# Kernel optimization log

Hardware: AMD Instinct MI355X
Metric: run time of the kernel (lower is better)

Reference implementation:

```python
import jax, jax.numpy as jnp
import numpy as np

EMBED_DIM = 1024
NUM_HEADS = 16
HEAD_DIM = 64
B, S = 4, 2048


def setup_inputs() -> dict:
    key = jax.random.key(0)
    ks = jax.random.split(key, 5)
    std = 0.02
    x = jax.random.normal(ks[0], (B, S, EMBED_DIM), dtype=jnp.float32)
    Wq = std * jax.random.normal(ks[1], (NUM_HEADS, EMBED_DIM, HEAD_DIM), dtype=jnp.float32)
    Wk = std * jax.random.normal(ks[2], (NUM_HEADS, EMBED_DIM, HEAD_DIM), dtype=jnp.float32)
    Wv = std * jax.random.normal(ks[3], (NUM_HEADS, EMBED_DIM, HEAD_DIM), dtype=jnp.float32)
    Wo = std * jax.random.normal(ks[4], (NUM_HEADS, HEAD_DIM, EMBED_DIM), dtype=jnp.float32)
    bq = jnp.zeros((NUM_HEADS, HEAD_DIM), dtype=jnp.float32)
    bk = jnp.zeros((NUM_HEADS, HEAD_DIM), dtype=jnp.float32)
    bv = jnp.zeros((NUM_HEADS, HEAD_DIM), dtype=jnp.float32)
    bo = jnp.zeros((EMBED_DIM,), dtype=jnp.float32)
    return {"x": x, "Wq": Wq, "bq": bq, "Wk": Wk, "bk": bk,
            "Wv": Wv, "bv": bv, "Wo": Wo, "bo": bo}


def reference(x, Wq, bq, Wk, bk, Wv, bv, Wo, bo):
    # q,k,v: [b, s, n, h]
    q = jnp.einsum('bsd,ndh->bsnh', x, Wq) + bq
    k = jnp.einsum('bsd,ndh->bsnh', x, Wk) + bk
    v = jnp.einsum('bsd,ndh->bsnh', x, Wv) + bv
    scale = 1.0 / (HEAD_DIM ** 0.5)
    # non-causal full attention matrix [b, n, s, t]
    attn = jnp.einsum('bsnh,btnh->bnst', q, k) * scale
    attn = jax.nn.softmax(attn, axis=-1)
    after = jnp.einsum('bnst,btnh->bsnh', attn, v)
    out = jnp.einsum('bsnh,nhd->bsd', after, Wo) + bo
    return out
```

## Files before the change

kernel.cpp:

```cpp
#include <hip/hip_runtime.h>

typedef __bf16 bf16;
typedef bf16 bf16x8 __attribute__((ext_vector_type(8)));
typedef bf16 bf16x4 __attribute__((ext_vector_type(4)));
typedef float f32x4 __attribute__((ext_vector_type(4)));

constexpr int Bb = 4, Ss = 2048, Dd = 1024, NH = 16, HD = 64;
constexpr int BS = Bb * Ss;
constexpr float CSC = 0.18033688011112042f;

__device__ __forceinline__ int sw(int row, int col) {
  return (row << 6) + (col ^ ((row & 7) << 3));
}

__device__ __forceinline__ void g2l16(const bf16* g, bf16* l) {
  __builtin_amdgcn_global_load_lds(
      (const __attribute__((address_space(1))) void*)g,
      (__attribute__((address_space(3))) void*)l, 16, 0, 0);
}

__global__ void convert_x(const float* __restrict__ x, bf16* __restrict__ xb) {
  int o = (blockIdx.x * 256 + threadIdx.x) * 4;
  f32x4 v = *(const f32x4*)&x[o];
  bf16x4 r = {(bf16)v[0], (bf16)v[1], (bf16)v[2], (bf16)v[3]};
  *(bf16x4*)&xb[o] = r;
}

__global__ void prep(const float* __restrict__ Wq, const float* __restrict__ Wk,
                     const float* __restrict__ Wv, const float* __restrict__ Wo,
                     const float* __restrict__ bq, const float* __restrict__ bk,
                     const float* __restrict__ bv,
                     bf16* __restrict__ WT_all, bf16* __restrict__ WoT,
                     float* __restrict__ bias_all) {
  __shared__ bf16 Ts[64 * 72];
  const int t = threadIdx.x;
  const int sel = blockIdx.y;
  if (sel < 3) {
    const float* W = (sel == 0) ? Wq : (sel == 1) ? Wk : Wv;
    float scale = (sel == 0) ? CSC : 1.0f;
    int head = blockIdx.x >> 4, dt = blockIdx.x & 15;
    const float* src = W + head * 65536 + dt * 64 * 64;
#pragma unroll
    for (int i = 0; i < 4; ++i) {
      int idx = i * 256 + t;
      int dr = idx >> 4, hc = (idx & 15) * 4;
      f32x4 v = *(const f32x4*)&src[dr * 64 + hc];
#pragma unroll
      for (int k = 0; k < 4; ++k) Ts[(hc + k) * 72 + dr] = (bf16)(v[k] * scale);
    }
    __syncthreads();
    bf16* dst = WT_all + (size_t)sel * 1048576 + (size_t)(head * 64) * 1024 + dt * 64;
#pragma unroll
    for (int i = 0; i < 2; ++i) {
      int idx = i * 256 + t;
      int hr = idx >> 3, ch = (idx & 7) * 8;
      *(bf16x8*)&dst[(size_t)hr * 1024 + ch] = *(const bf16x8*)&Ts[hr * 72 + ch];
    }
  } else if (sel == 3) {
    int ct = blockIdx.x >> 4, dt = blockIdx.x & 15;
    const float* src = Wo + (size_t)(ct * 64) * 1024 + dt * 64;
#pragma unroll
    for (int i = 0; i < 4; ++i) {
      int idx = i * 256 + t;
      int cr = idx >> 4, dc = (idx & 15) * 4;
      f32x4 v = *(const f32x4*)&src[(size_t)cr * 1024 + dc];
#pragma unroll
      for (int k = 0; k < 4; ++k) Ts[(dc + k) * 72 + cr] = (bf16)v[k];
    }
    __syncthreads();
    bf16* dst = WoT + (size_t)(dt * 64) * 1024 + ct * 64;
#pragma unroll
    for (int i = 0; i < 2; ++i) {
      int idx = i * 256 + t;
      int dr = idx >> 3, ch = (idx & 7) * 8;
      *(bf16x8*)&dst[(size_t)dr * 1024 + ch] = *(const bf16x8*)&Ts[dr * 72 + ch];
    }
  } else if (blockIdx.x == 0) {
    for (int j = t; j < 3072; j += 256) {
      int s2 = j >> 10;
      const float* bb = (s2 == 0) ? bq : (s2 == 1) ? bk : bv;
      bias_all[j] = bb[j & 1023] * (s2 == 0 ? CSC : 1.0f);
    }
  }
}

template <int EPI>
__global__ __launch_bounds__(256) void gemm128(const bf16* __restrict__ A,
                                               const bf16* __restrict__ BT,
                                               const float* __restrict__ bias,
                                               void* __restrict__ Cv, int ldc) {
  __shared__ __align__(16) bf16 As[128 * 64];
  __shared__ __align__(16) bf16 Bs[128 * 64];
  const int t = threadIdx.x;
  const int l = t & 63, q = l >> 4, lm = l & 15;
  const int w = t >> 6, wm = w & 1, wn = w >> 1;
  const int m0 = blockIdx.x * 128, n0 = blockIdx.y * 128;
  constexpr int K = 1024;
  int ro[4], co[4];
#pragma unroll
  for (int i = 0; i < 4; ++i) {
    int o = i * 256 + t;
    ro[i] = o >> 3;
    co[i] = ((o & 7) ^ ((o >> 3) & 7)) << 3;
  }
  const int lbase = (t & 192) * 8;
  f32x4 acc[4][4] = {};
  for (int k0 = 0; k0 < K; k0 += 64) {
    __syncthreads();
#pragma unroll
    for (int i = 0; i < 4; ++i)
      g2l16(&A[(size_t)(m0 + ro[i]) * K + k0 + co[i]], &As[i * 2048 + lbase]);
#pragma unroll
    for (int i = 0; i < 4; ++i)
      g2l16(&BT[(size_t)(n0 + ro[i]) * K + k0 + co[i]], &Bs[i * 2048 + lbase]);
    __syncthreads();
#pragma unroll
    for (int kh = 0; kh < 2; ++kh) {
      bf16x8 a[4], b[4];
#pragma unroll
      for (int i = 0; i < 4; ++i)
        a[i] = *(const bf16x8*)&As[sw(wm * 64 + i * 16 + lm, kh * 32 + q * 8)];
#pragma unroll
      for (int i = 0; i < 4; ++i)
        b[i] = *(const bf16x8*)&Bs[sw(wn * 64 + i * 16 + lm, kh * 32 + q * 8)];
#pragma unroll
      for (int mt = 0; mt < 4; ++mt)
#pragma unroll
        for (int nt = 0; nt < 4; ++nt)
          acc[mt][nt] = __builtin_amdgcn_mfma_f32_16x16x32_bf16(a[mt], b[nt], acc[mt][nt], 0, 0, 0);
    }
  }
  if (EPI == 1) {
    bf16* VT = (bf16*)Cv;
#pragma unroll
    for (int nt = 0; nt < 4; ++nt) {
      int sg = n0 + wn * 64 + nt * 16 + lm;
      size_t sb = (size_t)(sg >> 11) * 2097152 + (sg & 2047);
#pragma unroll
      for (int mt = 0; mt < 4; ++mt)
#pragma unroll
        for (int r = 0; r < 4; ++r) {
          int m = m0 + wm * 64 + mt * 16 + q * 4 + r;
          VT[sb + (size_t)(m >> 6) * 131072 + (size_t)(m & 63) * 2048] =
              (bf16)(acc[mt][nt][r] + bias[m]);
        }
    }
  } else {
#pragma unroll
    for (int nt = 0; nt < 4; ++nt) {
      int col = n0 + wn * 64 + nt * 16 + lm;
      float bb = bias[col];
#pragma unroll
      for (int mt = 0; mt < 4; ++mt) {
        int row = m0 + wm * 64 + mt * 16 + q * 4;
#pragma unroll
        for (int r = 0; r < 4; ++r) {
          if (EPI == 2)
            ((float*)Cv)[(size_t)(row + r) * ldc + col] = acc[mt][nt][r] + bb;
          else
            ((bf16*)Cv)[(size_t)(row + r) * ldc + col] = (bf16)(acc[mt][nt][r] + bb);
        }
      }
    }
  }
}

__global__ __launch_bounds__(256, 3) void attn(const bf16* __restrict__ QK,
                                               const bf16* __restrict__ VT,
                                               bf16* __restrict__ after) {
  __shared__ __align__(16) bf16 Ks[2][64 * 64];
  __shared__ __align__(16) bf16 Vs[2][64 * 64];
  __shared__ __align__(16) bf16 Ps[128 * 72];
  const int t = threadIdx.x;
  const int l = t & 63, q = l >> 4, lm = l & 15, w = t >> 6;
  const int f = blockIdx.x;
  const int bn = (f & 7) | ((f >> 7) << 3);
  const int s0 = ((f >> 3) & 15) * 128;
  const int b = bn >> 4, n = bn & 15;
  const bf16* Qb = QK + (size_t)(b * 2048) * 2048 + n * 64;
  const bf16* Kb = Qb + 1024;
  const bf16* Vtb = VT + (size_t)bn * 131072;
  int ro[4], co[4];
#pragma unroll
  for (int i = 0; i < 4; ++i) {
    int o = i * 256 + t;
    ro[i] = o >> 3;
    co[i] = ((o & 7) ^ ((o >> 3) & 7)) << 3;
  }
  const int lbase = (t & 192) * 8;
  bf16* Kflat = &Ks[0][0];
#pragma unroll
  for (int i = 0; i < 4; ++i)
    g2l16(&Qb[(size_t)(s0 + ro[i]) * 2048 + co[i]], Kflat + i * 2048 + lbase);
  __syncthreads();
  bf16x8 qa[2][2];
#pragma unroll
  for (int mt = 0; mt < 2; ++mt)
#pragma unroll
    for (int kh = 0; kh < 2; ++kh)
      qa[mt][kh] = *(const bf16x8*)&Kflat[sw(w * 32 + mt * 16 + lm, kh * 32 + q * 8)];
  __syncthreads();
#pragma unroll
  for (int i = 0; i < 2; ++i) {
    g2l16(&Kb[(size_t)ro[i] * 2048 + co[i]], &Ks[0][i * 2048 + lbase]);
    g2l16(&Vtb[(size_t)ro[i] * 2048 + co[i]], &Vs[0][i * 2048 + lbase]);
  }
  f32x4 o_acc[2][4] = {};
  f32x4 rsum[2] = {};
  const bf16x8 ones = {(bf16)1.f, (bf16)1.f, (bf16)1.f, (bf16)1.f,
                       (bf16)1.f, (bf16)1.f, (bf16)1.f, (bf16)1.f};
  for (int rd = 0; rd < 32; ++rd) {
    const int cur = rd & 1;
    __syncthreads();
    if (rd < 31) {
      int t0n = (rd + 1) * 64, nb = cur ^ 1;
#pragma unroll
      for (int i = 0; i < 2; ++i) {
        g2l16(&Kb[(size_t)(t0n + ro[i]) * 2048 + co[i]], &Ks[nb][i * 2048 + lbase]);
        g2l16(&Vtb[(size_t)ro[i] * 2048 + t0n + co[i]], &Vs[nb][i * 2048 + lbase]);
      }
    }
    f32x4 sc[2][4] = {};
#pragma unroll
    for (int kh = 0; kh < 2; ++kh) {
      bf16x8 kb[4];
#pragma unroll
      for (int c = 0; c < 4; ++c)
        kb[c] = *(const bf16x8*)&Ks[cur][sw(c * 16 + lm, kh * 32 + q * 8)];
#pragma unroll
      for (int mt = 0; mt < 2; ++mt)
#pragma unroll
        for (int c = 0; c < 4; ++c)
          sc[mt][c] = __builtin_amdgcn_mfma_f32_16x16x32_bf16(kb[c], qa[mt][kh], sc[mt][c], 0, 0, 0);
    }
#pragma unroll
    for (int mt = 0; mt < 2; ++mt) {
      int srow = w * 32 + mt * 16 + lm;
#pragma unroll
      for (int c = 0; c < 4; ++c) {
        bf16x4 pk;
#pragma unroll
        for (int r = 0; r < 4; ++r)
          pk[r] = (bf16)__builtin_amdgcn_exp2f(sc[mt][c][r]);
        *(bf16x4*)&Ps[srow * 72 + (c * 4 + q) * 4] = pk;
      }
    }
#pragma unroll
    for (int kh = 0; kh < 2; ++kh) {
      bf16x8 pa[2], vb[4];
#pragma unroll
      for (int mt = 0; mt < 2; ++mt)
        pa[mt] = *(const bf16x8*)&Ps[(w * 32 + mt * 16 + lm) * 72 + (kh * 8 + q * 2) * 4];
#pragma unroll
      for (int c = 0; c < 4; ++c)
        vb[c] = *(const bf16x8*)&Vs[cur][sw(c * 16 + lm, kh * 32 + q * 8)];
#pragma unroll
      for (int mt = 0; mt < 2; ++mt)
        rsum[mt] = __builtin_amdgcn_mfma_f32_16x16x32_bf16(pa[mt], ones, rsum[mt], 0, 0, 0);
#pragma unroll
      for (int mt = 0; mt < 2; ++mt)
#pragma unroll
        for (int c = 0; c < 4; ++c)
          o_acc[mt][c] = __builtin_amdgcn_mfma_f32_16x16x32_bf16(pa[mt], vb[c], o_acc[mt][c], 0, 0, 0);
    }
  }
#pragma unroll
  for (int mt = 0; mt < 2; ++mt)
#pragma unroll
    for (int r = 0; r < 4; ++r) {
      float inv = 1.f / rsum[mt][r];
      int srow = s0 + w * 32 + mt * 16 + q * 4 + r;
      size_t base = (size_t)(b * 2048 + srow) * 1024 + n * 64;
#pragma unroll
      for (int c = 0; c < 4; ++c)
        after[base + c * 16 + lm] = (bf16)(o_acc[mt][c][r] * inv);
    }
}

extern "C" void kernel_launch(void* const* d_in, const int* in_sizes, int n_in,
                              void* d_out, int out_size, void* d_ws, size_t ws_size,
                              hipStream_t stream) {
  const float* x  = (const float*)d_in[0];
  const float* Wq = (const float*)d_in[1];
  const float* bq = (const float*)d_in[2];
  const float* Wk = (const float*)d_in[3];
  const float* bk = (const float*)d_in[4];
  const float* Wv = (const float*)d_in[5];
  const float* bv = (const float*)d_in[6];
  const float* Wo = (const float*)d_in[7];
  const float* bo = (const float*)d_in[8];
  float* out = (float*)d_out;

  bf16* WT_all    = (bf16*)d_ws;
  bf16* WoT       = WT_all + (size_t)3072 * 1024;
  float* bias_all = (float*)(WoT + (size_t)1024 * 1024);
  bf16* xb        = (bf16*)(bias_all + 4096);
  bf16* QKb       = xb + (size_t)BS * Dd;
  bf16* VTb       = QKb + (size_t)BS * 2048;
  bf16* after     = VTb + (size_t)Bb * NH * HD * Ss;

  convert_x<<<dim3(BS * Dd / 1024), dim3(256), 0, stream>>>(x, xb);
  prep<<<dim3(256, 5), dim3(256), 0, stream>>>(Wq, Wk, Wv, Wo, bq, bk, bv,
                                               WT_all, WoT, bias_all);
  gemm128<0><<<dim3(64, 16), dim3(256), 0, stream>>>(xb, WT_all, bias_all, QKb, 2048);
  gemm128<1><<<dim3(8, 64), dim3(256), 0, stream>>>(WT_all + (size_t)2048 * 1024, xb,
                                                    bias_all + 2048, VTb, 0);
  attn<<<dim3(1024), dim3(256), 0, stream>>>(QKb, VTb, after);
  gemm128<2><<<dim3(64, 8), dim3(256), 0, stream>>>(after, WoT, bo, out, 1024);
}
```

Before: 290.5 us.

## Merge QK and V projection GEMMs into one launch with XCD-aware tile mapping

Fuses the separate QK and V projection GEMM launches into a single 1536-block kernel. Block indices are remapped so that blocks on the same XCD (bid&7) share weight column tiles, which should improve L2 reuse. The output GEMM gets the same XCD-aware mapping. The attention P-tile stride shrinks from 72 to 68, with P fragments read as two 8-byte loads to change the LDS bank pattern, at the cost of more LDS instructions.

```diff
diff --git a/kernel.cpp b/kernel.cpp
--- a/kernel.cpp
+++ b/kernel.cpp
@@ -8,6 +8,7 @@
 constexpr int Bb = 4, Ss = 2048, Dd = 1024, NH = 16, HD = 64;
 constexpr int BS = Bb * Ss;
 constexpr float CSC = 0.18033688011112042f;
+constexpr int PST = 68;
 
 __device__ __forceinline__ int sw(int row, int col) {
   return (row << 6) + (col ^ ((row & 7) << 3));
@@ -84,18 +85,13 @@
   }
 }
 
-template <int EPI>
-__global__ __launch_bounds__(256) void gemm128(const bf16* __restrict__ A,
-                                               const bf16* __restrict__ BT,
-                                               const float* __restrict__ bias,
-                                               void* __restrict__ Cv, int ldc) {
-  __shared__ __align__(16) bf16 As[128 * 64];
-  __shared__ __align__(16) bf16 Bs[128 * 64];
+__device__ __forceinline__ void gemm_core(const bf16* __restrict__ A,
+                                          const bf16* __restrict__ BT,
+                                          int m0, int n0, bf16* As, bf16* Bs,
+                                          f32x4 (&acc)[4][4]) {
   const int t = threadIdx.x;
   const int l = t & 63, q = l >> 4, lm = l & 15;
   const int w = t >> 6, wm = w & 1, wn = w >> 1;
-  const int m0 = blockIdx.x * 128, n0 = blockIdx.y * 128;
-  constexpr int K = 1024;
   int ro[4], co[4];
 #pragma unroll
   for (int i = 0; i < 4; ++i) {
@@ -104,15 +100,14 @@
     co[i] = ((o & 7) ^ ((o >> 3) & 7)) << 3;
   }
   const int lbase = (t & 192) * 8;
-  f32x4 acc[4][4] = {};
-  for (int k0 = 0; k0 < K; k0 += 64) {
+  for (int k0 = 0; k0 < 1024; k0 += 64) {
     __syncthreads();
 #pragma unroll
     for (int i = 0; i < 4; ++i)
-      g2l16(&A[(size_t)(m0 + ro[i]) * K + k0 + co[i]], &As[i * 2048 + lbase]);
+      g2l16(&A[(size_t)(m0 + ro[i]) * 1024 + k0 + co[i]], &As[i * 2048 + lbase]);
 #pragma unroll
     for (int i = 0; i < 4; ++i)
-      g2l16(&BT[(size_t)(n0 + ro[i]) * K + k0 + co[i]], &Bs[i * 2048 + lbase]);
+      g2l16(&BT[(size_t)(n0 + ro[i]) * 1024 + k0 + co[i]], &Bs[i * 2048 + lbase]);
     __syncthreads();
 #pragma unroll
     for (int kh = 0; kh < 2; ++kh) {
@@ -130,8 +125,37 @@
           acc[mt][nt] = __builtin_amdgcn_mfma_f32_16x16x32_bf16(a[mt], b[nt], acc[mt][nt], 0, 0, 0);
     }
   }
-  if (EPI == 1) {
-    bf16* VT = (bf16*)Cv;
+}
+
+__global__ __launch_bounds__(256) void gemm_qkv(const bf16* __restrict__ xb,
+                                                const bf16* __restrict__ WT,
+                                                const float* __restrict__ bias_all,
+                                                bf16* __restrict__ QKb,
+                                                bf16* __restrict__ VTb) {
+  __shared__ __align__(16) bf16 As[128 * 64];
+  __shared__ __align__(16) bf16 Bs[128 * 64];
+  const int bid = blockIdx.x;
+  const int t = threadIdx.x;
+  const int l = t & 63, q = l >> 4, lm = l & 15;
+  const int w = t >> 6, wm = w & 1, wn = w >> 1;
+  const bool vmode = bid >= 1024;
+  int m0, n0;
+  const bf16 *A, *BT;
+  if (!vmode) {
+    int xcd = bid & 7, idx = bid >> 3;
+    m0 = (idx >> 1) * 128;
+    n0 = (xcd * 2 + (idx & 1)) * 128;
+    A = xb; BT = WT;
+  } else {
+    int b2 = bid - 1024;
+    int xcd = b2 & 7, idx = b2 >> 3;
+    m0 = (idx >> 3) * 128;
+    n0 = (xcd * 8 + (idx & 7)) * 128;
+    A = WT + (size_t)2048 * 1024; BT = xb;
+  }
+  f32x4 acc[4][4] = {};
+  gemm_core(A, BT, m0, n0, As, Bs, acc);
+  if (vmode) {
 #pragma unroll
     for (int nt = 0; nt < 4; ++nt) {
       int sg = n0 + wn * 64 + nt * 16 + lm;
@@ -141,26 +165,50 @@
 #pragma unroll
         for (int r = 0; r < 4; ++r) {
           int m = m0 + wm * 64 + mt * 16 + q * 4 + r;
-          VT[sb + (size_t)(m >> 6) * 131072 + (size_t)(m & 63) * 2048] =
-              (bf16)(acc[mt][nt][r] + bias[m]);
+          VTb[sb + (size_t)(m >> 6) * 131072 + (size_t)(m & 63) * 2048] =
+              (bf16)(acc[mt][nt][r] + bias_all[2048 + m]);
         }
     }
   } else {
 #pragma unroll
     for (int nt = 0; nt < 4; ++nt) {
       int col = n0 + wn * 64 + nt * 16 + lm;
-      float bb = bias[col];
+      float bb = bias_all[col];
 #pragma unroll
       for (int mt = 0; mt < 4; ++mt) {
         int row = m0 + wm * 64 + mt * 16 + q * 4;
 #pragma unroll
-        for (int r = 0; r < 4; ++r) {
-          if (EPI == 2)
-            ((float*)Cv)[(size_t)(row + r) * ldc + col] = acc[mt][nt][r] + bb;
-          else
-            ((bf16*)Cv)[(size_t)(row + r) * ldc + col] = (bf16)(acc[mt][nt][r] + bb);
-        }
+        for (int r = 0; r < 4; ++r)
+          QKb[(size_t)(row + r) * 2048 + col] = (bf16)(acc[mt][nt][r] + bb);
       }
+    }
+  }
+}
+
+__global__ __launch_bounds__(256) void gemm_out(const bf16* __restrict__ after,
+                                                const bf16* __restrict__ WoT,
+                                                const float* __restrict__ bo,
+                                                float* __restrict__ out) {
+  __shared__ __align__(16) bf16 As[128 * 64];
+  __shared__ __align__(16) bf16 Bs[128 * 64];
+  const int bid = blockIdx.x;
+  const int t = threadIdx.x;
+  const int l = t & 63, q = l >> 4, lm = l & 15;
+  const int w = t >> 6, wm = w & 1, wn = w >> 1;
+  const int xcd = bid & 7, idx = bid >> 3;
+  const int n0 = xcd * 128, m0 = idx * 128;
+  f32x4 acc[4][4] = {};
+  gemm_core(after, WoT, m0, n0, As, Bs, acc);
+#pragma unroll
+  for (int nt = 0; nt < 4; ++nt) {
+    int col = n0 + wn * 64 + nt * 16 + lm;
+    float bb = bo[col];
+#pragma unroll
+    for (int mt = 0; mt < 4; ++mt) {
+      int row = m0 + wm * 64 + mt * 16 + q * 4;
+#pragma unroll
+      for (int r = 0; r < 4; ++r)
+        out[(size_t)(row + r) * 1024 + col] = acc[mt][nt][r] + bb;
     }
   }
 }
@@ -170,7 +218,7 @@
                                                bf16* __restrict__ after) {
   __shared__ __align__(16) bf16 Ks[2][64 * 64];
   __shared__ __align__(16) bf16 Vs[2][64 * 64];
-  __shared__ __align__(16) bf16 Ps[128 * 72];
+  __shared__ __align__(16) bf16 Ps[128 * PST];
   const int t = threadIdx.x;
   const int l = t & 63, q = l >> 4, lm = l & 15, w = t >> 6;
   const int f = blockIdx.x;
@@ -242,18 +290,23 @@
 #pragma unroll
         for (int r = 0; r < 4; ++r)
           pk[r] = (bf16)__builtin_amdgcn_exp2f(sc[mt][c][r]);
-        *(bf16x4*)&Ps[srow * 72 + (c * 4 + q) * 4] = pk;
+        *(bf16x4*)&Ps[srow * PST + (c * 4 + q) * 4] = pk;
       }
     }
 #pragma unroll
     for (int kh = 0; kh < 2; ++kh) {
-      bf16x8 pa[2], vb[4];
-#pragma unroll
-      for (int mt = 0; mt < 2; ++mt)
-        pa[mt] = *(const bf16x8*)&Ps[(w * 32 + mt * 16 + lm) * 72 + (kh * 8 + q * 2) * 4];
+      bf16x8 vb[4];
 #pragma unroll
       for (int c = 0; c < 4; ++c)
         vb[c] = *(const bf16x8*)&Vs[cur][sw(c * 16 + lm, kh * 32 + q * 8)];
+      bf16x8 pa[2];
+#pragma unroll
+      for (int mt = 0; mt < 2; ++mt) {
+        int srow = w * 32 + mt * 16 + lm;
+        bf16x4 lo = *(const bf16x4*)&Ps[srow * PST + (kh * 8 + q * 2) * 4];
+        bf16x4 hi = *(const bf16x4*)&Ps[srow * PST + (kh * 8 + q * 2) * 4 + 4];
+        pa[mt] = __builtin_shufflevector(lo, hi, 0, 1, 2, 3, 4, 5, 6, 7);
+      }
 #pragma unroll
       for (int mt = 0; mt < 2; ++mt)
         rsum[mt] = __builtin_amdgcn_mfma_f32_16x16x32_bf16(pa[mt], ones, rsum[mt], 0, 0, 0);
@@ -302,9 +355,7 @@
   convert_x<<<dim3(BS * Dd / 1024), dim3(256), 0, stream>>>(x, xb);
   prep<<<dim3(256, 5), dim3(256), 0, stream>>>(Wq, Wk, Wv, Wo, bq, bk, bv,
                                                WT_all, WoT, bias_all);
-  gemm128<0><<<dim3(64, 16), dim3(256), 0, stream>>>(xb, WT_all, bias_all, QKb, 2048);
-  gemm128<1><<<dim3(8, 64), dim3(256), 0, stream>>>(WT_all + (size_t)2048 * 1024, xb,
-                                                    bias_all + 2048, VTb, 0);
+  gemm_qkv<<<dim3(1536), dim3(256), 0, stream>>>(xb, WT_all, bias_all, QKb, VTb);
   attn<<<dim3(1024), dim3(256), 0, stream>>>(QKb, VTb, after);
-  gemm128<2><<<dim3(64, 8), dim3(256), 0, stream>>>(after, WoT, bo, out, 1024);
-}
+  gemm_out<<<dim3(512), dim3(256), 0, stream>>>(after, WoT, bo, out);
+}
```

Result: faster. 277.0 us (-4.7%).
